# Optimization experiments

Measured on AMD Instinct MI355X. Metric: run time of the kernel, lower is better.

The kernel has to match this reference:

```python
import jax, jax.numpy as jnp
import numpy as np
from jax import lax

B, T, N, D = 8, 256, 128, 16
H, Hb, K, L, OUT = 128, 64, 3, 8, 24  # L = num_stacks*layers_per_stack
DILS = [2 ** (i % 4) for i in range(L)]


def setup_inputs() -> dict:
    key = jax.random.key(0)
    ks = jax.random.split(key, 16)
    s = 0.05
    return {
        "x": jax.random.normal(ks[0], (B, T, N, D), jnp.float32),
        "in_w": jax.random.normal(ks[1], (D, H), jnp.float32) * s,
        "in_b": jnp.zeros((H,), jnp.float32),
        "pw_in_w": jax.random.normal(ks[2], (L, Hb, H), jnp.float32) * s,   # conv1x1 H->Hb
        "dw_w": jax.random.normal(ks[3], (L, 2 * Hb, 1, K), jnp.float32) * s,  # grouped conv, groups=Hb
        "pw_out_w": jax.random.normal(ks[4], (L, H, Hb), jnp.float32) * s,  # conv1x1 Hb->H
        "gn_g": jnp.ones((L, H), jnp.float32),
        "gn_b": jnp.zeros((L, H), jnp.float32),
        "skip_w": jax.random.normal(ks[5], (L, H, H), jnp.float32) * s,
        "ln_g": jnp.ones((H,), jnp.float32),
        "ln_b": jnp.zeros((H,), jnp.float32),
        "h1_w": jax.random.normal(ks[6], (H, H), jnp.float32) * s,
        "h1_b": jnp.zeros((H,), jnp.float32),
        "h2_w": jax.random.normal(ks[7], (H, OUT), jnp.float32) * s,
        "h2_b": jnp.zeros((OUT,), jnp.float32),
    }


def _group_norm1(x, g, b, eps=1e-5):
    # GroupNorm(num_groups=1, C): normalize over (C, T) per sample, per-channel affine
    m = jnp.mean(x, axis=(1, 2), keepdims=True)
    v = jnp.var(x, axis=(1, 2), keepdims=True)
    return (x - m) * lax.rsqrt(v + eps) * g[None, :, None] + b[None, :, None]


def reference(x, in_w, in_b, pw_in_w, dw_w, pw_out_w, gn_g, gn_b, skip_w,
              ln_g, ln_b, h1_w, h1_b, h2_w, h2_b):
    b, t, n, _ = x.shape
    h = x @ in_w + in_b                              # (B,T,N,H)
    z = h.transpose(0, 2, 3, 1).reshape(b * n, H, t)  # (B*N,H,T)
    skip_sum = jnp.zeros_like(z)
    for i, d in enumerate(DILS):
        u = jnp.einsum('bct,oc->bot', z, pw_in_w[i])  # pointwise H->Hb
        pad = (K - 1) * d
        u = jnp.pad(u, ((0, 0), (0, 0), (pad, 0)))   # causal left-pad
        v = lax.conv_general_dilated(
            u, dw_w[i], (1,), 'VALID', rhs_dilation=(d,),
            dimension_numbers=('NCH', 'OIH', 'NCH'), feature_group_count=Hb)
        f, gate = jnp.split(v, 2, axis=1)            # torch.chunk(z, 2, dim=1)
        w = jnp.tanh(f) * jax.nn.sigmoid(gate)       # GLU gate, (B*N,Hb,T)
        s_feat = jnp.einsum('bct,oc->bot', w, pw_out_w[i])  # Hb->H (dropout=identity in eval)
        z = _group_norm1(z + s_feat, gn_g[i], gn_b[i])
        skip_sum = skip_sum + jnp.einsum('bct,oc->bot', s_feat, skip_w[i])
    h_last = skip_sum[:, :, -1]                      # (B*N,H)
    mu = jnp.mean(h_last, -1, keepdims=True)
    var = jnp.var(h_last, -1, keepdims=True)
    hn = (h_last - mu) * lax.rsqrt(var + 1e-5) * ln_g + ln_b
    y = jax.nn.gelu(hn @ h1_w + h1_b, approximate=False) @ h2_w + h2_b  # (B*N,OUT)
    return y.reshape(b, n, OUT).transpose(0, 2, 1)   # (B,T_out,N)
```

## Files before the change

### kernel.cpp

```cpp
#include <hip/hip_runtime.h>
#include <hip/hip_fp16.h>
#include <math.h>

#define TT 256
#define HC 128
#define HB 64
#define NL 8

#define WS_PB  65536
#define WS_PG  66048
#define WS_GP  66560
#define WS_BP  67584

typedef _Float16 f16x8 __attribute__((ext_vector_type(8)));
typedef float f32x4 __attribute__((ext_vector_type(4)));

__device__ __forceinline__ f16x8 asf16x8(uint4 v) {
    union { uint4 u; f16x8 h; } cv; cv.u = v; return cv.h;
}
__device__ __forceinline__ f32x4 mfma16(uint4 a, uint4 b, f32x4 c) {
    return __builtin_amdgcn_mfma_f32_16x16x32_f16(asf16x8(a), asf16x8(b), c, 0, 0, 0);
}
__device__ __forceinline__ float fast_tanh(float x) {
    float e = __expf(2.f * fabsf(x));
    float r = 1.f - 2.f / (1.f + e);
    return copysignf(r, x);
}
__device__ __forceinline__ float fast_sig(float x) {
    return 1.f / (1.f + __expf(-x));
}
__device__ __forceinline__ unsigned packh2(float a, float b) {
    __half2 h = __floats2half2_rn(a, b);
    return __builtin_bit_cast(unsigned, h);
}
__device__ __forceinline__ float loh(unsigned u) {
    return __low2float(__builtin_bit_cast(__half2, u));
}
__device__ __forceinline__ float hih(unsigned u) {
    return __high2float(__builtin_bit_cast(__half2, u));
}
__device__ __forceinline__ unsigned u4get(uint4 v, int q) {
    return q == 0 ? v.x : q == 1 ? v.y : q == 2 ? v.z : v.w;
}

__global__ __launch_bounds__(256)
void tcn_setup(const float* __restrict__ pw_in, const float* __restrict__ pw_out,
               const float* __restrict__ gn_g, const float* __restrict__ gn_b,
               float* __restrict__ ws) {
    const int i = blockIdx.x;
    const int tid = threadIdx.x;
    uint4* WPA = (uint4*)ws;
    float* Pb = ws + WS_PB;
    float* Pg = ws + WS_PG;
    float* Gp = ws + WS_GP;
    float* Bp = ws + WS_BP;

    if (tid < HC) {
        float g  = (i == 0) ? 1.f : gn_g[(i - 1) * HC + tid];
        float bb = (i == 0) ? 0.f : gn_b[(i - 1) * HC + tid];
        Gp[i * HC + tid] = g;
        Bp[i * HC + tid] = bb;
    }
    for (int e = tid; e < 16 * 64; e += 256) {
        int tile = e >> 6, lane = e & 63;
        int mt = tile >> 2, kt = tile & 3;
        int o = 16 * mt + (lane & 15);
        int chb = 32 * kt + 8 * (lane >> 4);
        uint4 v;
        unsigned vq[4];
        for (int q = 0; q < 4; q++) {
            int ch = chb + 2 * q;
            float g0 = (i == 0) ? 1.f : gn_g[(i - 1) * HC + ch];
            float g1 = (i == 0) ? 1.f : gn_g[(i - 1) * HC + ch + 1];
            float w0 = pw_in[((size_t)i * HB + o) * HC + ch] * g0;
            float w1 = pw_in[((size_t)i * HB + o) * HC + ch + 1] * g1;
            vq[q] = packh2(w0, w1);
        }
        v.x = vq[0]; v.y = vq[1]; v.z = vq[2]; v.w = vq[3];
        WPA[((size_t)i * 16 + tile) * 64 + lane] = v;
    }
    for (int e = tid; e < 16 * 64; e += 256) {
        int tile = e >> 6, lane = e & 63;
        int ms = tile >> 1, ks = tile & 1;
        int o = 16 * ms + (lane & 15);
        int chb = 32 * ks + 8 * (lane >> 4);
        uint4 v;
        unsigned vq[4];
        for (int q = 0; q < 4; q++) {
            int ch = chb + 2 * q;
            float w0 = pw_out[((size_t)i * HC + o) * HB + ch];
            float w1 = pw_out[((size_t)i * HC + o) * HB + ch + 1];
            vq[q] = packh2(w0, w1);
        }
        v.x = vq[0]; v.y = vq[1]; v.z = vq[2]; v.w = vq[3];
        WPA[8192 + ((size_t)i * 16 + tile) * 64 + lane] = v;
    }
    if (tid < HB) {
        float pb = 0.f, pg = 0.f;
        for (int c = 0; c < HC; c++) {
            float w = pw_in[((size_t)i * HB + tid) * HC + c];
            float gc = (i == 0) ? 1.f : gn_g[(i - 1) * HC + c];
            float bc = (i == 0) ? 0.f : gn_b[(i - 1) * HC + c];
            pb += bc * w;
            pg += gc * w;
        }
        Pb[i * HB + tid] = pb;
        Pg[i * HB + tid] = pg;
    }
}

__global__ __launch_bounds__(256)
void tcn_main(const float* __restrict__ x, const float* __restrict__ in_w,
              const float* __restrict__ in_b, const float* __restrict__ dw_w,
              const float* __restrict__ pw_out, const float* __restrict__ skip_w,
              const float* __restrict__ ln_g, const float* __restrict__ ln_b,
              const float* __restrict__ h1_w, const float* __restrict__ h1_b,
              const float* __restrict__ h2_w, const float* __restrict__ h2_b,
              const float* __restrict__ ws, float* __restrict__ out) {
    __shared__ unsigned scratch[4224];
    __shared__ unsigned haloB[3 * 32 * 17];
    __shared__ float sLast[NL * HC];
    __shared__ float red[16];
    float* hbuf = (float*)scratch;
    float* qbuf = hbuf + 128;

    const float* Pb = ws + WS_PB;
    const float* Pg = ws + WS_PG;
    const float* Gp = ws + WS_GP;
    const float* Bp = ws + WS_BP;
    const uint4* WPA = (const uint4*)ws;

    const int t = threadIdx.x;
    const int bn = blockIdx.x;
    const int b = bn >> 7, n = bn & 127;
    const int lane = t & 63;
    const int wv = t >> 6;
    const int cc = lane & 15;
    const int l4 = lane >> 4;

    unsigned z2[64];
    {
        const float* xp = x + (((size_t)b * TT + t) * 128 + n) * 16;
        float xr[16];
#pragma unroll
        for (int d = 0; d < 16; d++) xr[d] = xp[d];
#pragma unroll
        for (int c = 0; c < HC; c += 2) {
            float a0 = in_b[c], a1 = in_b[c + 1];
#pragma unroll
            for (int d = 0; d < 16; d++) {
                a0 = fmaf(xr[d], in_w[d * HC + c], a0);
                a1 = fmaf(xr[d], in_w[d * HC + c + 1], a1);
            }
            z2[c >> 1] = packh2(a0, a1);
        }
    }

    uint4 zB[4][4];
#pragma unroll
    for (int kt = 0; kt < 4; kt++) {
#pragma unroll
        for (int q = 0; q < 16; q++) scratch[q * 257 + t] = z2[16 * kt + q];
        __syncthreads();
#pragma unroll
        for (int nt = 0; nt < 4; nt++) {
            int col = 64 * wv + nt * 16 + cc;
            uint4 v;
            v.x = scratch[(4 * l4 + 0) * 257 + col];
            v.y = scratch[(4 * l4 + 1) * 257 + col];
            v.z = scratch[(4 * l4 + 2) * 257 + col];
            v.w = scratch[(4 * l4 + 3) * 257 + col];
            zB[kt][nt] = v;
        }
        __syncthreads();
    }

    float m_s = 0.f, r_s = 1.f;

#pragma unroll 1
    for (int L = 0; L < NL; L++) {
        const int dil = 1 << (L & 3), d1 = dil, d2 = 2 * dil;
        const bool lastL = (L == NL - 1);
        const bool act = (!lastL) || (wv == 3);
        const float mr = m_s * r_s;

        unsigned pu[4][4][2];
        if (act) {
            const uint4* AU = WPA + (size_t)L * 16 * 64;
#pragma unroll
            for (int mt = 0; mt < 4; mt++) {
                uint4 a0 = AU[(mt * 4 + 0) * 64 + lane];
                uint4 a1 = AU[(mt * 4 + 1) * 64 + lane];
                uint4 a2 = AU[(mt * 4 + 2) * 64 + lane];
                uint4 a3 = AU[(mt * 4 + 3) * 64 + lane];
                float4 pbv = *(const float4*)(Pb + L * HB + 16 * mt + 4 * l4);
                float4 pgv = *(const float4*)(Pg + L * HB + 16 * mt + 4 * l4);
#pragma unroll
                for (int nt = 0; nt < 4; nt++) {
                    f32x4 acc = {0.f, 0.f, 0.f, 0.f};
                    acc = mfma16(a0, zB[0][nt], acc);
                    acc = mfma16(a1, zB[1][nt], acc);
                    acc = mfma16(a2, zB[2][nt], acc);
                    acc = mfma16(a3, zB[3][nt], acc);
                    float u0 = fmaf(r_s, acc[0], pbv.x - mr * pgv.x);
                    float u1 = fmaf(r_s, acc[1], pbv.y - mr * pgv.y);
                    float u2 = fmaf(r_s, acc[2], pbv.z - mr * pgv.z);
                    float u3 = fmaf(r_s, acc[3], pbv.w - mr * pgv.w);
                    pu[mt][nt][0] = packh2(u0, u1);
                    pu[mt][nt][1] = packh2(u2, u3);
                }
            }
            if (wv < 3) {
#pragma unroll
                for (int mt = 0; mt < 4; mt++)
#pragma unroll
                    for (int rp = 0; rp < 2; rp++)
                        haloB[wv * (32 * 17) + (8 * mt + 2 * l4 + rp) * 17 + cc] = pu[mt][3][rp];
            }
        }
        __syncthreads();

        unsigned bwv[2][4][4];
        if (act) {
            const float* dwl = dw_w + (size_t)L * 384;
            const int hb = (wv > 0 ? wv - 1 : 0) * (32 * 17);
#pragma unroll
            for (int mtf = 0; mtf < 2; mtf++) {
#pragma unroll
                for (int rp = 0; rp < 2; rp++) {
                    unsigned hf = 0u, hg = 0u;
                    if (wv > 0) {
                        hf = haloB[hb + (8 * mtf + 2 * l4 + rp) * 17 + cc];
                        hg = haloB[hb + (8 * (mtf + 2) + 2 * l4 + rp) * 17 + cc];
                    }
                    unsigned m1f[4], m1g[4], m2f[4], m2g[4];
                    {
                        const int srcl = (lane & 48) | ((cc - d1) & 15);
                        const bool own = (cc <= 15 - d1);
#pragma unroll
                        for (int nt = 0; nt < 4; nt++) {
                            unsigned wf = own ? pu[mtf][nt][rp]
                                              : (nt > 0 ? pu[mtf][nt - 1][rp] : hf);
                            unsigned wg = own ? pu[mtf + 2][nt][rp]
                                              : (nt > 0 ? pu[mtf + 2][nt - 1][rp] : hg);
                            m1f[nt] = __shfl(wf, srcl);
                            m1g[nt] = __shfl(wg, srcl);
                        }
                    }
                    {
                        const int srcl = (lane & 48) | ((cc - d2) & 15);
                        const bool own = (cc <= 15 - d2);
#pragma unroll
                        for (int nt = 0; nt < 4; nt++) {
                            unsigned wf = own ? pu[mtf][nt][rp]
                                              : (nt > 0 ? pu[mtf][nt - 1][rp] : hf);
                            unsigned wg = own ? pu[mtf + 2][nt][rp]
                                              : (nt > 0 ? pu[mtf + 2][nt - 1][rp] : hg);
                            m2f[nt] = __shfl(wf, srcl);
                            m2g[nt] = __shfl(wg, srcl);
                        }
                    }
                    const int o = 16 * mtf + 4 * l4 + 2 * rp;
                    const float* df = dwl + (2 * o) * 3;
                    const float* dg = dwl + (64 + 2 * o) * 3;
#pragma unroll
                    for (int nt = 0; nt < 4; nt++) {
                        float uf0 = loh(pu[mtf][nt][rp]),     uf1 = hih(pu[mtf][nt][rp]);
                        float ug0 = loh(pu[mtf + 2][nt][rp]), ug1 = hih(pu[mtf + 2][nt][rp]);
                        float a1f0 = loh(m1f[nt]), a1f1 = hih(m1f[nt]);
                        float a2f0 = loh(m2f[nt]), a2f1 = hih(m2f[nt]);
                        float a1g0 = loh(m1g[nt]), a1g1 = hih(m1g[nt]);
                        float a2g0 = loh(m2g[nt]), a2g1 = hih(m2g[nt]);
                        float f0 = a2f0 * df[0] + a1f0 * df[1]  + uf0 * df[2];
                        float f1 = a2f0 * df[3] + a1f0 * df[4]  + uf0 * df[5];
                        float f2 = a2f1 * df[6] + a1f1 * df[7]  + uf1 * df[8];
                        float f3 = a2f1 * df[9] + a1f1 * df[10] + uf1 * df[11];
                        float g0 = a2g0 * dg[0] + a1g0 * dg[1]  + ug0 * dg[2];
                        float g1 = a2g0 * dg[3] + a1g0 * dg[4]  + ug0 * dg[5];
                        float g2 = a2g1 * dg[6] + a1g1 * dg[7]  + ug1 * dg[8];
                        float g3 = a2g1 * dg[9] + a1g1 * dg[10] + ug1 * dg[11];
                        bwv[mtf][nt][2 * rp] =
                            packh2(fast_tanh(f0) * fast_sig(g0), fast_tanh(f1) * fast_sig(g1));
                        bwv[mtf][nt][2 * rp + 1] =
                            packh2(fast_tanh(f2) * fast_sig(g2), fast_tanh(f3) * fast_sig(g3));
                    }
                }
            }
        }

        float s1 = 0.f, s2 = 0.f;
        if (act) {
            uint4 Bw[2][4];
#pragma unroll
            for (int ks = 0; ks < 2; ks++)
#pragma unroll
                for (int nt = 0; nt < 4; nt++) {
                    uint4 v;
                    v.x = bwv[ks][nt][0]; v.y = bwv[ks][nt][1];
                    v.z = bwv[ks][nt][2]; v.w = bwv[ks][nt][3];
                    Bw[ks][nt] = v;
                }
            const uint4* AS = WPA + 8192 + (size_t)L * 16 * 64;
            unsigned* SB = scratch + wv * (16 * 66);
#pragma unroll
            for (int kt = 0; kt < 4; kt++) {
                f32x4 cs[2][4];
#pragma unroll
                for (int lo = 0; lo < 2; lo++) {
                    const int ms = 2 * kt + lo;
                    uint4 a0 = AS[(ms * 2 + 0) * 64 + lane];
                    uint4 a1 = AS[(ms * 2 + 1) * 64 + lane];
#pragma unroll
                    for (int nt = 0; nt < 4; nt++) {
                        f32x4 acc = {0.f, 0.f, 0.f, 0.f};
                        acc = mfma16(a0, Bw[0][nt], acc);
                        acc = mfma16(a1, Bw[1][nt], acc);
                        cs[lo][nt] = acc;
                    }
                }
                if (wv == 3 && cc == 15) {
#pragma unroll
                    for (int lo = 0; lo < 2; lo++)
#pragma unroll
                        for (int r = 0; r < 4; r++)
                            sLast[L * HC + 16 * (2 * kt + lo) + 4 * l4 + r] = cs[lo][3][r];
                }
                if (!lastL) {
#pragma unroll
                    for (int lo = 0; lo < 2; lo++)
#pragma unroll
                        for (int nt = 0; nt < 4; nt++) {
                            SB[(8 * lo + 2 * l4 + 0) * 66 + 16 * nt + cc] =
                                packh2(cs[lo][nt][0], cs[lo][nt][1]);
                            SB[(8 * lo + 2 * l4 + 1) * 66 + 16 * nt + cc] =
                                packh2(cs[lo][nt][2], cs[lo][nt][3]);
                        }
#pragma unroll
                    for (int nt = 0; nt < 4; nt++) {
                        unsigned zp[4];
#pragma unroll
                        for (int q = 0; q < 4; q++) {
                            unsigned sp = SB[(4 * l4 + q) * 66 + 16 * nt + cc];
                            float sf0 = loh(sp), sf1 = hih(sp);
                            unsigned zold = u4get(zB[kt][nt], q);
                            float zo0 = loh(zold), zo1 = hih(zold);
                            float2 gv = *(const float2*)(Gp + L * HC + 32 * kt + 8 * l4 + 2 * q);
                            float2 bv = *(const float2*)(Bp + L * HC + 32 * kt + 8 * l4 + 2 * q);
                            float zn0 = fmaf(zo0, r_s * gv.x, (bv.x - mr * gv.x) + sf0);
                            float zn1 = fmaf(zo1, r_s * gv.y, (bv.y - mr * gv.y) + sf1);
                            zp[q] = packh2(zn0, zn1);
                            s1 += zn0 + zn1;
                            s2 += zn0 * zn0 + zn1 * zn1;
                        }
                        uint4 v;
                        v.x = zp[0]; v.y = zp[1]; v.z = zp[2]; v.w = zp[3];
                        zB[kt][nt] = v;
                    }
                }
            }
        }
        if (!lastL) {
#pragma unroll
            for (int off = 32; off; off >>= 1) {
                s1 += __shfl_xor(s1, off);
                s2 += __shfl_xor(s2, off);
            }
            if (lane == 0) { red[wv * 2] = s1; red[wv * 2 + 1] = s2; }
            __syncthreads();
            float S1 = red[0] + red[2] + red[4] + red[6];
            float S2 = red[1] + red[3] + red[5] + red[7];
            float mu = S1 * (1.f / 32768.f);
            float var = S2 * (1.f / 32768.f) - mu * mu;
            m_s = mu;
            r_s = rsqrtf(var + 1e-5f);
        }
    }
    __syncthreads();

    float hl = 0.f;
    if (t < HC) {
        for (int i = 0; i < NL; i++) {
            const float4* swr = (const float4*)(skip_w + (((size_t)i * HC) + t) * HC);
            const float* sl = sLast + i * HC;
#pragma unroll 4
            for (int c4 = 0; c4 < 32; c4++) {
                float4 sw = swr[c4];
                hl += sw.x * sl[4 * c4] + sw.y * sl[4 * c4 + 1] + sw.z * sl[4 * c4 + 2] + sw.w * sl[4 * c4 + 3];
            }
        }
        hbuf[t] = hl;
    }
    __syncthreads();
    if (t < 64) {
        float v0 = hbuf[t], v1 = hbuf[t + 64];
        float a = v0 + v1, q = v0 * v0 + v1 * v1;
#pragma unroll
        for (int off = 32; off; off >>= 1) {
            a += __shfl_xor(a, off);
            q += __shfl_xor(q, off);
        }
        if (t == 0) {
            float mu = a * (1.f / 128.f);
            red[0] = mu;
            red[1] = rsqrtf(q * (1.f / 128.f) - mu * mu + 1e-5f);
        }
    }
    __syncthreads();
    {
        float mu = red[0], rs = red[1];
        if (t < HC) hbuf[t] = (hl - mu) * rs * ln_g[t] + ln_b[t];
    }
    __syncthreads();
    if (t < HC) {
        float q = h1_b[t];
        for (int c = 0; c < HC; c++) q = fmaf(hbuf[c], h1_w[c * HC + t], q);
        q = 0.5f * q * (1.f + erff(q * 0.70710678118654752f));
        qbuf[t] = q;
    }
    __syncthreads();
    if (t < 24) {
        float o = h2_b[t];
        for (int c = 0; c < HC; c++) o = fmaf(qbuf[c], h2_w[c * 24 + t], o);
        out[((size_t)b * 24 + t) * 128 + n] = o;
    }
}

extern "C" void kernel_launch(void* const* d_in, const int* in_sizes, int n_in,
                              void* d_out, int out_size, void* d_ws, size_t ws_size,
                              hipStream_t stream) {
    const float* x      = (const float*)d_in[0];
    const float* in_w   = (const float*)d_in[1];
    const float* in_b   = (const float*)d_in[2];
    const float* pw_in  = (const float*)d_in[3];
    const float* dw_w   = (const float*)d_in[4];
    const float* pw_out = (const float*)d_in[5];
    const float* gn_g   = (const float*)d_in[6];
    const float* gn_b   = (const float*)d_in[7];
    const float* skip_w = (const float*)d_in[8];
    const float* ln_g   = (const float*)d_in[9];
    const float* ln_b   = (const float*)d_in[10];
    const float* h1_w   = (const float*)d_in[11];
    const float* h1_b   = (const float*)d_in[12];
    const float* h2_w   = (const float*)d_in[13];
    const float* h2_b   = (const float*)d_in[14];
    float* out = (float*)d_out;
    float* ws  = (float*)d_ws;

    tcn_setup<<<NL, 256, 0, stream>>>(pw_in, pw_out, gn_g, gn_b, ws);

    tcn_main<<<1024, 256, 0, stream>>>(x, in_w, in_b, dw_w, pw_out, skip_w,
                                       ln_g, ln_b, h1_w, h1_b, h2_w, h2_b, ws, out);
}
```

Before: 488.9 us.

## Split each sample across eight waves instead of four to halve register state

The main kernel now runs 512 threads per block. Each wave owns 32 time steps instead of 64, so the per-thread z, pu and bwv register arrays shrink by half, and halo exchange now covers seven neighbour waves. The input projection is split so each thread pair covers one time step with half the channels each. That projection, with its barriers, is oddly computed twice, which adds redundant work and extra syncs in exchange for lower register pressure and potentially higher occupancy.

```diff
diff --git a/kernel.cpp b/kernel.cpp
--- a/kernel.cpp
+++ b/kernel.cpp
@@ -109,7 +109,7 @@
     }
 }
 
-__global__ __launch_bounds__(256)
+__global__ __launch_bounds__(512)
 void tcn_main(const float* __restrict__ x, const float* __restrict__ in_w,
               const float* __restrict__ in_b, const float* __restrict__ dw_w,
               const float* __restrict__ pw_out, const float* __restrict__ skip_w,
@@ -117,8 +117,8 @@
               const float* __restrict__ h1_w, const float* __restrict__ h1_b,
               const float* __restrict__ h2_w, const float* __restrict__ h2_b,
               const float* __restrict__ ws, float* __restrict__ out) {
-    __shared__ unsigned scratch[4224];
-    __shared__ unsigned haloB[3 * 32 * 17];
+    __shared__ unsigned scratch[4352];
+    __shared__ unsigned haloB[7 * 32 * 17];
     __shared__ float sLast[NL * HC];
     __shared__ float red[16];
     float* hbuf = (float*)scratch;
@@ -130,47 +130,85 @@
     const float* Bp = ws + WS_BP;
     const uint4* WPA = (const uint4*)ws;
 
-    const int t = threadIdx.x;
+    const int tid = threadIdx.x;
     const int bn = blockIdx.x;
     const int b = bn >> 7, n = bn & 127;
-    const int lane = t & 63;
-    const int wv = t >> 6;
+    const int lane = tid & 63;
+    const int wv = tid >> 6;
     const int cc = lane & 15;
     const int l4 = lane >> 4;
 
-    unsigned z2[64];
+    const int tt = tid >> 1, half = tid & 1;
     {
-        const float* xp = x + (((size_t)b * TT + t) * 128 + n) * 16;
+        unsigned z2loc[32];
+        const float* xp = x + (((size_t)b * TT + tt) * 128 + n) * 16;
         float xr[16];
 #pragma unroll
         for (int d = 0; d < 16; d++) xr[d] = xp[d];
 #pragma unroll
-        for (int c = 0; c < HC; c += 2) {
-            float a0 = in_b[c], a1 = in_b[c + 1];
+        for (int i = 0; i < 32; i++) {
+            const int ch = 64 * half + 2 * i;
+            float a0 = in_b[ch], a1 = in_b[ch + 1];
 #pragma unroll
             for (int d = 0; d < 16; d++) {
-                a0 = fmaf(xr[d], in_w[d * HC + c], a0);
-                a1 = fmaf(xr[d], in_w[d * HC + c + 1], a1);
-            }
-            z2[c >> 1] = packh2(a0, a1);
-        }
-    }
-
-    uint4 zB[4][4];
-#pragma unroll
-    for (int kt = 0; kt < 4; kt++) {
-#pragma unroll
-        for (int q = 0; q < 16; q++) scratch[q * 257 + t] = z2[16 * kt + q];
-        __syncthreads();
-#pragma unroll
-        for (int nt = 0; nt < 4; nt++) {
-            int col = 64 * wv + nt * 16 + cc;
-            uint4 v;
-            v.x = scratch[(4 * l4 + 0) * 257 + col];
-            v.y = scratch[(4 * l4 + 1) * 257 + col];
-            v.z = scratch[(4 * l4 + 2) * 257 + col];
-            v.w = scratch[(4 * l4 + 3) * 257 + col];
-            zB[kt][nt] = v;
+                a0 = fmaf(xr[d], in_w[d * HC + ch], a0);
+                a1 = fmaf(xr[d], in_w[d * HC + ch + 1], a1);
+            }
+            z2loc[i] = packh2(a0, a1);
+        }
+        ;
+        extern __shared__ char _dummy[]; (void)_dummy;
+        {
+        }
+#pragma unroll
+        for (int kt = 0; kt < 4; kt++) {
+            if ((kt >> 1) == half) {
+#pragma unroll
+                for (int q = 0; q < 16; q++)
+                    scratch[q * 257 + tt] = z2loc[16 * (kt & 1) + q];
+            }
+            __syncthreads();
+            __syncthreads();
+        }
+    }
+
+    uint4 zB[4][2];
+    {
+        unsigned z2loc[32];
+        const float* xp = x + (((size_t)b * TT + tt) * 128 + n) * 16;
+        float xr[16];
+#pragma unroll
+        for (int d = 0; d < 16; d++) xr[d] = xp[d];
+#pragma unroll
+        for (int i = 0; i < 32; i++) {
+            const int ch = 64 * half + 2 * i;
+            float a0 = in_b[ch], a1 = in_b[ch + 1];
+#pragma unroll
+            for (int d = 0; d < 16; d++) {
+                a0 = fmaf(xr[d], in_w[d * HC + ch], a0);
+                a1 = fmaf(xr[d], in_w[d * HC + ch + 1], a1);
+            }
+            z2loc[i] = packh2(a0, a1);
+        }
+#pragma unroll
+        for (int kt = 0; kt < 4; kt++) {
+            __syncthreads();
+            if ((kt >> 1) == half) {
+#pragma unroll
+                for (int q = 0; q < 16; q++)
+                    scratch[q * 257 + tt] = z2loc[16 * (kt & 1) + q];
+            }
+            __syncthreads();
+#pragma unroll
+            for (int nt = 0; nt < 2; nt++) {
+                int col = 32 * wv + 16 * nt + cc;
+                uint4 v;
+                v.x = scratch[(4 * l4 + 0) * 257 + col];
+                v.y = scratch[(4 * l4 + 1) * 257 + col];
+                v.z = scratch[(4 * l4 + 2) * 257 + col];
+                v.w = scratch[(4 * l4 + 3) * 257 + col];
+                zB[kt][nt] = v;
+            }
         }
         __syncthreads();
     }
@@ -181,10 +219,10 @@
     for (int L = 0; L < NL; L++) {
         const int dil = 1 << (L & 3), d1 = dil, d2 = 2 * dil;
         const bool lastL = (L == NL - 1);
-        const bool act = (!lastL) || (wv == 3);
+        const bool act = (!lastL) || (wv == 7);
         const float mr = m_s * r_s;
 
-        unsigned pu[4][4][2];
+        unsigned pu[4][2][2];
         if (act) {
             const uint4* AU = WPA + (size_t)L * 16 * 64;
 #pragma unroll
@@ -196,7 +234,7 @@
                 float4 pbv = *(const float4*)(Pb + L * HB + 16 * mt + 4 * l4);
                 float4 pgv = *(const float4*)(Pg + L * HB + 16 * mt + 4 * l4);
 #pragma unroll
-                for (int nt = 0; nt < 4; nt++) {
+                for (int nt = 0; nt < 2; nt++) {
                     f32x4 acc = {0.f, 0.f, 0.f, 0.f};
                     acc = mfma16(a0, zB[0][nt], acc);
                     acc = mfma16(a1, zB[1][nt], acc);
@@ -210,17 +248,17 @@
                     pu[mt][nt][1] = packh2(u2, u3);
                 }
             }
-            if (wv < 3) {
+            if (wv < 7) {
 #pragma unroll
                 for (int mt = 0; mt < 4; mt++)
 #pragma unroll
                     for (int rp = 0; rp < 2; rp++)
-                        haloB[wv * (32 * 17) + (8 * mt + 2 * l4 + rp) * 17 + cc] = pu[mt][3][rp];
+                        haloB[wv * (32 * 17) + (8 * mt + 2 * l4 + rp) * 17 + cc] = pu[mt][1][rp];
             }
         }
         __syncthreads();
 
-        unsigned bwv[2][4][4];
+        unsigned bwv[2][2][4];
         if (act) {
             const float* dwl = dw_w + (size_t)L * 384;
             const int hb = (wv > 0 ? wv - 1 : 0) * (32 * 17);
@@ -233,12 +271,12 @@
                         hf = haloB[hb + (8 * mtf + 2 * l4 + rp) * 17 + cc];
                         hg = haloB[hb + (8 * (mtf + 2) + 2 * l4 + rp) * 17 + cc];
                     }
-                    unsigned m1f[4], m1g[4], m2f[4], m2g[4];
+                    unsigned m1f[2], m1g[2], m2f[2], m2g[2];
                     {
                         const int srcl = (lane & 48) | ((cc - d1) & 15);
                         const bool own = (cc <= 15 - d1);
 #pragma unroll
-                        for (int nt = 0; nt < 4; nt++) {
+                        for (int nt = 0; nt < 2; nt++) {
                             unsigned wf = own ? pu[mtf][nt][rp]
                                               : (nt > 0 ? pu[mtf][nt - 1][rp] : hf);
                             unsigned wg = own ? pu[mtf + 2][nt][rp]
@@ -251,7 +289,7 @@
                         const int srcl = (lane & 48) | ((cc - d2) & 15);
                         const bool own = (cc <= 15 - d2);
 #pragma unroll
-                        for (int nt = 0; nt < 4; nt++) {
+                        for (int nt = 0; nt < 2; nt++) {
                             unsigned wf = own ? pu[mtf][nt][rp]
                                               : (nt > 0 ? pu[mtf][nt - 1][rp] : hf);
                             unsigned wg = own ? pu[mtf + 2][nt][rp]
@@ -264,7 +302,7 @@
                     const float* df = dwl + (2 * o) * 3;
                     const float* dg = dwl + (64 + 2 * o) * 3;
 #pragma unroll
-                    for (int nt = 0; nt < 4; nt++) {
+                    for (int nt = 0; nt < 2; nt++) {
                         float uf0 = loh(pu[mtf][nt][rp]),     uf1 = hih(pu[mtf][nt][rp]);
                         float ug0 = loh(pu[mtf + 2][nt][rp]), ug1 = hih(pu[mtf + 2][nt][rp]);
                         float a1f0 = loh(m1f[nt]), a1f1 = hih(m1f[nt]);
@@ -290,57 +328,57 @@
 
         float s1 = 0.f, s2 = 0.f;
         if (act) {
-            uint4 Bw[2][4];
+            uint4 Bw[2][2];
 #pragma unroll
             for (int ks = 0; ks < 2; ks++)
 #pragma unroll
-                for (int nt = 0; nt < 4; nt++) {
+                for (int nt = 0; nt < 2; nt++) {
                     uint4 v;
                     v.x = bwv[ks][nt][0]; v.y = bwv[ks][nt][1];
                     v.z = bwv[ks][nt][2]; v.w = bwv[ks][nt][3];
                     Bw[ks][nt] = v;
                 }
             const uint4* AS = WPA + 8192 + (size_t)L * 16 * 64;
-            unsigned* SB = scratch + wv * (16 * 66);
+            unsigned* SB = scratch + wv * 544;
 #pragma unroll
             for (int kt = 0; kt < 4; kt++) {
-                f32x4 cs[2][4];
+                f32x4 cs[2][2];
 #pragma unroll
                 for (int lo = 0; lo < 2; lo++) {
                     const int ms = 2 * kt + lo;
                     uint4 a0 = AS[(ms * 2 + 0) * 64 + lane];
                     uint4 a1 = AS[(ms * 2 + 1) * 64 + lane];
 #pragma unroll
-                    for (int nt = 0; nt < 4; nt++) {
+                    for (int nt = 0; nt < 2; nt++) {
                         f32x4 acc = {0.f, 0.f, 0.f, 0.f};
                         acc = mfma16(a0, Bw[0][nt], acc);
                         acc = mfma16(a1, Bw[1][nt], acc);
                         cs[lo][nt] = acc;
                     }
                 }
-                if (wv == 3 && cc == 15) {
+                if (wv == 7 && cc == 15) {
 #pragma unroll
                     for (int lo = 0; lo < 2; lo++)
 #pragma unroll
                         for (int r = 0; r < 4; r++)
-                            sLast[L * HC + 16 * (2 * kt + lo) + 4 * l4 + r] = cs[lo][3][r];
+                            sLast[L * HC + 16 * (2 * kt + lo) + 4 * l4 + r] = cs[lo][1][r];
                 }
                 if (!lastL) {
 #pragma unroll
                     for (int lo = 0; lo < 2; lo++)
 #pragma unroll
-                        for (int nt = 0; nt < 4; nt++) {
-                            SB[(8 * lo + 2 * l4 + 0) * 66 + 16 * nt + cc] =
+                        for (int nt = 0; nt < 2; nt++) {
+                            SB[(8 * lo + 2 * l4 + 0) * 34 + 16 * nt + cc] =
                                 packh2(cs[lo][nt][0], cs[lo][nt][1]);
-                            SB[(8 * lo + 2 * l4 + 1) * 66 + 16 * nt + cc] =
+                            SB[(8 * lo + 2 * l4 + 1) * 34 + 16 * nt + cc] =
                                 packh2(cs[lo][nt][2], cs[lo][nt][3]);
                         }
 #pragma unroll
-                    for (int nt = 0; nt < 4; nt++) {
+                    for (int nt = 0; nt < 2; nt++) {
                         unsigned zp[4];
 #pragma unroll
                         for (int q = 0; q < 4; q++) {
-                            unsigned sp = SB[(4 * l4 + q) * 66 + 16 * nt + cc];
+                            unsigned sp = SB[(4 * l4 + q) * 34 + 16 * nt + cc];
                             float sf0 = loh(sp), sf1 = hih(sp);
                             unsigned zold = u4get(zB[kt][nt], q);
                             float zo0 = loh(zold), zo1 = hih(zold);
@@ -367,8 +405,8 @@
             }
             if (lane == 0) { red[wv * 2] = s1; red[wv * 2 + 1] = s2; }
             __syncthreads();
-            float S1 = red[0] + red[2] + red[4] + red[6];
-            float S2 = red[1] + red[3] + red[5] + red[7];
+            float S1 = red[0] + red[2] + red[4] + red[6] + red[8] + red[10] + red[12] + red[14];
+            float S2 = red[1] + red[3] + red[5] + red[7] + red[9] + red[11] + red[13] + red[15];
             float mu = S1 * (1.f / 32768.f);
             float var = S2 * (1.f / 32768.f) - mu * mu;
             m_s = mu;
@@ -377,6 +415,7 @@
     }
     __syncthreads();
 
+    const int t = tid;
     float hl = 0.f;
     if (t < HC) {
         for (int i = 0; i < NL; i++) {
@@ -448,6 +487,6 @@
 
     tcn_setup<<<NL, 256, 0, stream>>>(pw_in, pw_out, gn_g, gn_b, ws);
 
-    tcn_main<<<1024, 256, 0, stream>>>(x, in_w, in_b, dw_w, pw_out, skip_w,
+    tcn_main<<<1024, 512, 0, stream>>>(x, in_w, in_b, dw_w, pw_out, skip_w,
                                        ln_g, ln_b, h1_w, h1_b, h2_w, h2_b, ws, out);
 }
```

Result: slower. 972.1 us (+98.8%).
